# Kernel tuning notes

Hardware: AMD Instinct MI355X
Metric: run time of the kernel (lower is better)

## Reference

```python
import jax, jax.numpy as jnp
import numpy as np
from jax import lax

N, S, F_IN = 50000, 16, 64
HID, HEADS = 128, 4
C = HID // HEADS  # 32
E = 1600000
NEG_SLOPE = 0.2


def setup_inputs() -> dict:
    key = jax.random.key(0)
    ks = jax.random.split(key, 16)
    sc = lambda *sh: 1.0 / np.sqrt(sh[-1])
    inp = {}
    inp['node_features_sequence'] = jax.random.normal(ks[0], (N, S, F_IN), dtype=jnp.float32)
    inp['edge_index'] = jax.random.randint(ks[1], (2, E), 0, N, dtype=jnp.int64)
    # GRU params (single layer, order r,z,n as in torch)
    inp['gru_w_ih'] = jax.random.normal(ks[2], (3 * HID, F_IN), jnp.float32) * sc(F_IN)
    inp['gru_w_hh'] = jax.random.normal(ks[3], (3 * HID, HID), jnp.float32) * sc(HID)
    inp['gru_b_ih'] = jax.random.normal(ks[4], (3 * HID,), jnp.float32) * 0.01
    inp['gru_b_hh'] = jax.random.normal(ks[5], (3 * HID,), jnp.float32) * 0.01
    # GAT layer 1
    inp['gat1_w'] = jax.random.normal(ks[6], (HID, HID), jnp.float32) * sc(HID)
    inp['gat1_a_src'] = jax.random.normal(ks[7], (HEADS, C), jnp.float32) * sc(C)
    inp['gat1_a_dst'] = jax.random.normal(ks[8], (HEADS, C), jnp.float32) * sc(C)
    inp['gat1_b'] = jnp.zeros((HID,), jnp.float32)
    # GAT layer 2
    inp['gat2_w'] = jax.random.normal(ks[9], (HID, HID), jnp.float32) * sc(HID)
    inp['gat2_a_src'] = jax.random.normal(ks[10], (HEADS, C), jnp.float32) * sc(C)
    inp['gat2_a_dst'] = jax.random.normal(ks[11], (HEADS, C), jnp.float32) * sc(C)
    inp['gat2_b'] = jnp.zeros((HID,), jnp.float32)
    # classifier
    inp['clf_w'] = jax.random.normal(ks[12], (1, HID), jnp.float32) * sc(HID)
    inp['clf_b'] = jnp.zeros((1,), jnp.float32)
    return inp


def gru_last(xs, w_ih, w_hh, b_ih, b_hh):
    # xs: [N, S, F] -> last hidden [N, H]
    n, _, _ = xs.shape
    h_dim = w_hh.shape[1]
    gi_all = jnp.einsum('nsf,gf->nsg', xs, w_ih) + b_ih  # [N,S,3H]
    gi_all = jnp.swapaxes(gi_all, 0, 1)  # [S,N,3H]

    def step(h, gi):
        gh = h @ w_hh.T + b_hh
        i_r, i_z, i_n = jnp.split(gi, 3, axis=-1)
        h_r, h_z, h_n = jnp.split(gh, 3, axis=-1)
        r = jax.nn.sigmoid(i_r + h_r)
        z = jax.nn.sigmoid(i_z + h_z)
        nn_ = jnp.tanh(i_n + r * h_n)
        h_new = (1.0 - z) * nn_ + z * h
        return h_new, None

    h0 = jnp.zeros((n, h_dim), xs.dtype)
    h_last, _ = lax.scan(step, h0, gi_all)
    return h_last


def gat_layer(x, src, dst, w, a_src, a_dst, b):
    # x: [N, HID]; PyG GATConv with add_self_loops, concat heads
    n = x.shape[0]
    h = (x @ w.T).reshape(n, HEADS, C)  # [N,H,C]
    a_s = jnp.einsum('nhc,hc->nh', h, a_src)  # [N,H]
    a_d = jnp.einsum('nhc,hc->nh', h, a_dst)
    e = jax.nn.leaky_relu(a_s[src] + a_d[dst], NEG_SLOPE)  # [E',H]
    m = jax.ops.segment_max(e, dst, num_segments=n)
    m = jnp.where(jnp.isfinite(m), m, 0.0)
    ex = jnp.exp(e - m[dst])
    denom = jax.ops.segment_sum(ex, dst, num_segments=n)
    alpha = ex / (denom[dst] + 1e-16)  # [E',H]
    msg = h[src] * alpha[:, :, None]  # [E',H,C]
    out = jax.ops.segment_sum(msg, dst, num_segments=n)  # [N,H,C]
    return out.reshape(n, HEADS * C) + b


def reference(node_features_sequence, edge_index,
              gru_w_ih, gru_w_hh, gru_b_ih, gru_b_hh,
              gat1_w, gat1_a_src, gat1_a_dst, gat1_b,
              gat2_w, gat2_a_src, gat2_a_dst, gat2_b,
              clf_w, clf_b):
    n = node_features_sequence.shape[0]
    # add self loops once (same structure for both layers)
    loops = jnp.arange(n, dtype=edge_index.dtype)
    src = jnp.concatenate([edge_index[0], loops])
    dst = jnp.concatenate([edge_index[1], loops])

    x = gru_last(node_features_sequence, gru_w_ih, gru_w_hh, gru_b_ih, gru_b_hh)
    x = jax.nn.elu(gat_layer(x, src, dst, gat1_w, gat1_a_src, gat1_a_dst, gat1_b))
    x = jax.nn.elu(gat_layer(x, src, dst, gat2_w, gat2_a_src, gat2_a_dst, gat2_b))
    return jax.nn.sigmoid(x @ clf_w.T + clf_b)  # [N,1]
```

## Files before the change

### kernel.cpp

```cpp
#include <hip/hip_runtime.h>
#include <hip/hip_bf16.h>
#include <hip/hip_fp16.h>
#include <math.h>

#define N_NODES 50000
#define NP      50048
#define SEQ     16
#define FIN     64
#define HID     128
#define NEDGE   1600000
#define NB_SCAN 196
#define AGG_CAP 96

typedef __attribute__((ext_vector_type(8))) short short8;
typedef __attribute__((ext_vector_type(4))) float f32x4;

__device__ __forceinline__ float lrelu02(float v) { return v > 0.f ? v : 0.2f * v; }
__device__ __forceinline__ float frcp(float v) { return __builtin_amdgcn_rcpf(v); }
__device__ __forceinline__ float ex2(float v) { return __builtin_amdgcn_exp2f(v); }
__device__ __forceinline__ float sigmoidf_(float v) { return frcp(1.f + __expf(-v)); }
__device__ __forceinline__ float eluf_(float v) { return v > 0.f ? v : (__expf(v) - 1.f); }

__device__ __forceinline__ unsigned bfpk(float lo, float hi) {
    union { __hip_bfloat162 h; unsigned u; } c;
    c.h = __float22bfloat162_rn(make_float2(lo, hi));
    return c.u;
}
__device__ __forceinline__ unsigned hfpk(float lo, float hi) {
    union { __half2 h; unsigned u; } c;
    c.h = __float22half2_rn(make_float2(lo, hi));
    return c.u;
}
__device__ __forceinline__ float2 h2f2(unsigned u) {
    union { unsigned u; __half2 h; } c;
    c.u = u;
    return __half22float2(c.h);
}
__device__ __forceinline__ short8 pack8s(float4 a, float4 b, float s) {
    union { short8 sv; unsigned u[4]; } r;
    r.u[0] = bfpk(a.x * s, a.y * s); r.u[1] = bfpk(a.z * s, a.w * s);
    r.u[2] = bfpk(b.x * s, b.y * s); r.u[3] = bfpk(b.z * s, b.w * s);
    return r.sv;
}

#define BAR() do { asm volatile("s_waitcnt lgkmcnt(0)" ::: "memory"); \
                   __builtin_amdgcn_s_barrier(); } while (0)

__global__ __launch_bounds__(512, 2) void gru_fused(
    const float* __restrict__ x,
    const float* __restrict__ w_ih,
    const float* __restrict__ w_hh,
    const float* __restrict__ b_ih,
    const float* __restrict__ b_hh,
    float* __restrict__ hout)
{
    __shared__ __align__(16) short hA[2][2][32][136];
    __shared__ __align__(16) short xB[2][2][32][72];

    const int tid  = threadIdx.x;
    const int wave = tid >> 6;
    const int lane = tid & 63;
    const int q    = lane >> 4;
    const int rl   = lane & 15;
    const int n0   = blockIdx.x * 64;
    const int ch   = wave * 16 + rl;

    const float S1 = 1.44269504088896341f;
    const float S2 = 2.88539008177792682f;
    short8 whhf[3][4];
    short8 wihf[3][2];
#pragma unroll
    for (int g = 0; g < 3; g++) {
        const float gs = (g == 2) ? S2 : S1;
        int row = g * 128 + ch;
#pragma unroll
        for (int kc = 0; kc < 4; kc++) {
            const float* p = w_hh + row * HID + kc * 32 + q * 8;
            whhf[g][kc] = pack8s(*(const float4*)p, *(const float4*)(p + 4), gs);
        }
#pragma unroll
        for (int kc = 0; kc < 2; kc++) {
            const float* p = w_ih + row * FIN + kc * 32 + q * 8;
            wihf[g][kc] = pack8s(*(const float4*)p, *(const float4*)(p + 4), gs);
        }
    }

    const float br  = (b_ih[ch] + b_hh[ch]) * S1;
    const float bz  = (b_ih[128 + ch] + b_hh[128 + ch]) * S1;
    const float bin = b_ih[256 + ch] * S2;
    const float bhn = b_hh[256 + ch] * S2;

    const int sn = tid >> 4;
    const int sk = (tid & 15) * 4;
    int g0n = n0 + sn;      if (g0n > N_NODES - 1) g0n = N_NODES - 1;
    int g1n = n0 + 32 + sn; if (g1n > N_NODES - 1) g1n = N_NODES - 1;
    const float* xs0 = x + (size_t)g0n * SEQ * FIN + sk;
    const float* xs1 = x + (size_t)g1n * SEQ * FIN + sk;

    float hreg[2][2][4];
#pragma unroll
    for (int g = 0; g < 2; g++)
#pragma unroll
        for (int mt = 0; mt < 2; mt++)
#pragma unroll
            for (int r = 0; r < 4; r++) hreg[g][mt][r] = 0.f;

    f32x4 accr[2][2], accz[2][2], accin[2][2], acchn[2][2];
    float4 xh[2];

    {
        float4 v = *(const float4*)(xs0);
        int2 pv;
        pv.x = (int)bfpk(v.x, v.y);
        pv.y = (int)bfpk(v.z, v.w);
        *(int2*)&xB[0][0][sn][sk] = pv;
    }
    xh[1] = *(const float4*)(xs1);
    BAR();

#define GATE_BLOCK(B, PG, DO_HW, HWB)                                             \
    {                                                                             \
        _Pragma("unroll")                                                         \
        for (int mt = 0; mt < 2; mt++) {                                          \
            float rg[4], zg[4], et[4];                                            \
            _Pragma("unroll")                                                     \
            for (int r = 0; r < 4; r++) {                                         \
                float er  = ex2(fminf(-(accr[B][mt][r] + br), 60.f));             \
                float ezv = ex2(fminf(-(accz[B][mt][r] + bz), 60.f));             \
                float dr = er + 1.f, dz = ezv + 1.f;                              \
                float ip = frcp(dr * dz);                                         \
                rg[r] = dz * ip; zg[r] = dr * ip;                                 \
                float ap = accin[B][mt][r] + bin + rg[r] * (acchn[B][mt][r] + bhn); \
                et[r] = ex2(fminf(ap, 120.f));                                    \
            }                                                                     \
            _Pragma("unroll")                                                     \
            for (int pr = 0; pr < 2; pr++) {                                      \
                float dd0 = et[2 * pr] + 1.f, dd1 = et[2 * pr + 1] + 1.f;         \
                float ipt = frcp(dd0 * dd1);                                      \
                float nn0 = 1.f - 2.f * (ipt * dd1);                              \
                float nn1 = 1.f - 2.f * (ipt * dd0);                              \
                float h0 = zg[2 * pr]     * (hreg[PG][mt][2 * pr]     - nn0) + nn0; \
                float h1 = zg[2 * pr + 1] * (hreg[PG][mt][2 * pr + 1] - nn1) + nn1; \
                hreg[PG][mt][2 * pr] = h0; hreg[PG][mt][2 * pr + 1] = h1;         \
            }                                                                     \
            if (DO_HW) {                                                          \
                unsigned u01 = bfpk(hreg[PG][mt][0], hreg[PG][mt][1]);            \
                unsigned u23 = bfpk(hreg[PG][mt][2], hreg[PG][mt][3]);            \
                const int nb = mt * 16 + q * 4;                                   \
                hA[PG][HWB][nb + 0][ch] = (short)(u01 & 0xFFFF);                  \
                hA[PG][HWB][nb + 1][ch] = (short)(u01 >> 16);                     \
                hA[PG][HWB][nb + 2][ch] = (short)(u23 & 0xFFFF);                  \
                hA[PG][HWB][nb + 3][ch] = (short)(u23 >> 16);                     \
            }                                                                     \
        }                                                                         \
    }

#define GRU_PHASE(G, PG, DO_GATE, HWB, DO_HW, DO_XW, XWB, XPTR)                   \
    {                                                                             \
        short8 xf[2][2], hf[2][4];                                                \
        _Pragma("unroll")                                                         \
        for (int mt = 0; mt < 2; mt++)                                            \
            _Pragma("unroll")                                                     \
            for (int kc = 0; kc < 2; kc++)                                        \
                xf[mt][kc] = *(const short8*)&xB[G][t & 1][mt * 16 + rl][kc * 32 + q * 8]; \
        if (t > 0) {                                                              \
            _Pragma("unroll")                                                     \
            for (int mt = 0; mt < 2; mt++)                                        \
                _Pragma("unroll")                                                 \
                for (int kc = 0; kc < 4; kc++)                                    \
                    hf[mt][kc] = *(const short8*)&hA[G][(t - 1) & 1][mt * 16 + rl][kc * 32 + q * 8]; \
        }                                                                         \
        if (t + 1 < SEQ) xh[G] = *(const float4*)(XPTR + (t + 1) * FIN);          \
        _Pragma("unroll")                                                         \
        for (int mt = 0; mt < 2; mt++) {                                          \
            accr[G][mt]  = __builtin_amdgcn_mfma_f32_16x16x32_bf16(xf[mt][0], wihf[0][0], (f32x4)0.f, 0, 0, 0); \
            accz[G][mt]  = __builtin_amdgcn_mfma_f32_16x16x32_bf16(xf[mt][0], wihf[1][0], (f32x4)0.f, 0, 0, 0); \
            accin[G][mt] = __builtin_amdgcn_mfma_f32_16x16x32_bf16(xf[mt][0], wihf[2][0], (f32x4)0.f, 0, 0, 0); \
            accr[G][mt]  = __builtin_amdgcn_mfma_f32_16x16x32_bf16(xf[mt][1], wihf[0][1], accr[G][mt], 0, 0, 0); \
            accz[G][mt]  = __builtin_amdgcn_mfma_f32_16x16x32_bf16(xf[mt][1], wihf[1][1], accz[G][mt], 0, 0, 0); \
            accin[G][mt] = __builtin_amdgcn_mfma_f32_16x16x32_bf16(xf[mt][1], wihf[2][1], accin[G][mt], 0, 0, 0); \
            if (t > 0) {                                                          \
                acchn[G][mt] = __builtin_amdgcn_mfma_f32_16x16x32_bf16(hf[mt][0], whhf[2][0], (f32x4)0.f, 0, 0, 0); \
                _Pragma("unroll")                                                 \
                for (int kc = 0; kc < 4; kc++) {                                  \
                    accr[G][mt]  = __builtin_amdgcn_mfma_f32_16x16x32_bf16(hf[mt][kc], whhf[0][kc], accr[G][mt], 0, 0, 0);  \
                    accz[G][mt]  = __builtin_amdgcn_mfma_f32_16x16x32_bf16(hf[mt][kc], whhf[1][kc], accz[G][mt], 0, 0, 0);  \
                }                                                                 \
                _Pragma("unroll")                                                 \
                for (int kc = 1; kc < 4; kc++)                                    \
                    acchn[G][mt] = __builtin_amdgcn_mfma_f32_16x16x32_bf16(hf[mt][kc], whhf[2][kc], acchn[G][mt], 0, 0, 0); \
            } else {                                                              \
                acchn[G][mt] = (f32x4)0.f;                                        \
            }                                                                     \
        }                                                                         \
        if (DO_GATE) GATE_BLOCK(PG, PG, DO_HW, HWB);                              \
        if (DO_XW) {                                                              \
            int2 pv;                                                              \
            pv.x = (int)bfpk(xh[PG].x, xh[PG].y);                                 \
            pv.y = (int)bfpk(xh[PG].z, xh[PG].w);                                 \
            *(int2*)&xB[PG][XWB][sn][sk] = pv;                                    \
        }                                                                         \
        BAR();                                                                    \
    }

    for (int t = 0; t < SEQ; t++) {
        GRU_PHASE(0, 1, (t > 0), ((t - 1) & 1), (t > 0), 1, (t & 1), xs0)
        GRU_PHASE(1, 0, 1, (t & 1), (t + 1 < SEQ), (t + 1 < SEQ), ((t + 1) & 1), xs1)
    }
#undef GRU_PHASE

    GATE_BLOCK(1, 1, 0, 0);
#undef GATE_BLOCK

#pragma unroll
    for (int g = 0; g < 2; g++)
#pragma unroll
        for (int mt = 0; mt < 2; mt++)
#pragma unroll
            for (int r = 0; r < 4; r++)
                hout[(size_t)(n0 + g * 32 + mt * 16 + q * 4 + r) * HID + ch] = hreg[g][mt][r];
}

__global__ void prep_weights(const float* __restrict__ g1w, const float* __restrict__ g2w,
                             float* __restrict__ g1T, float* __restrict__ g2T)
{
    int i = blockIdx.x * 256 + threadIdx.x;
    if (i < 128 * 128) {
        int k = i >> 7, g = i & 127;
        g1T[i] = g1w[g * 128 + k];
        g2T[i] = g2w[g * 128 + k];
    }
}

__global__ void count_edges(const int* __restrict__ dst, int* __restrict__ deg, int e)
{
    int i = blockIdx.x * 256 + threadIdx.x;
    if (i < e) atomicAdd(&deg[dst[i]], 1);
}

__device__ __forceinline__ int block_scan_inc(int v)
{
    int tid = threadIdx.x, lane = tid & 63, w = tid >> 6;
#pragma unroll
    for (int off = 1; off < 64; off <<= 1) {
        int tmp = __shfl_up(v, off, 64);
        if (lane >= off) v += tmp;
    }
    __shared__ int wsum[4];
    if (lane == 63) wsum[w] = v;
    __syncthreads();
    int add = 0;
    for (int i = 0; i < w; i++) add += wsum[i];
    return v + add;
}

__global__ void scan_block_sums(const int* __restrict__ deg, int* __restrict__ bsum, int n)
{
    int i = blockIdx.x * 256 + threadIdx.x;
    int v = (i < n) ? deg[i] : 0;
#pragma unroll
    for (int off = 32; off >= 1; off >>= 1) v += __shfl_xor(v, off, 64);
    __shared__ int ws[4];
    if ((threadIdx.x & 63) == 0) ws[threadIdx.x >> 6] = v;
    __syncthreads();
    if (threadIdx.x == 0) bsum[blockIdx.x] = ws[0] + ws[1] + ws[2] + ws[3];
}

__global__ void scan_bsum(int* __restrict__ bsum, int nb)
{
    int tid = threadIdx.x;
    int v = (tid < nb) ? bsum[tid] : 0;
    v = block_scan_inc(v);
    if (tid < nb) bsum[tid] = v;
}

__global__ void scan_final(const int* __restrict__ deg, const int* __restrict__ bsum,
                           int* __restrict__ rp, int n)
{
    int i = blockIdx.x * 256 + threadIdx.x;
    int v = (i < n) ? deg[i] : 0;
    int s = block_scan_inc(v);
    int add = (blockIdx.x > 0) ? bsum[blockIdx.x - 1] : 0;
    if (i < n) rp[i + 1] = s + add;
    if (i == 0) rp[0] = 0;
}

__global__ void fill_edges(const int* __restrict__ src, const int* __restrict__ dst,
                           const int* __restrict__ rp, int* __restrict__ cur,
                           int* __restrict__ col, int e)
{
    int i = blockIdx.x * 256 + threadIdx.x;
    if (i < e) {
        int d = dst[i];
        int pos = atomicAdd(&cur[d], 1);
        col[rp[d] + pos] = src[i];
    }
}

__global__ __launch_bounds__(256) void proj_attn(
    const float* __restrict__ x, const float* __restrict__ wT,
    const float* __restrict__ a_src, const float* __restrict__ a_dst,
    unsigned* __restrict__ hph, float* __restrict__ as_, float* __restrict__ ad_)
{
    __shared__ float xt[32][33];
    __shared__ float wt[32][128];
    __shared__ float ot[32][132];
    const int tid = threadIdx.x;
    const int tx = tid & 7;
    const int ty = tid >> 3;
    const int n0 = blockIdx.x * 32;
    float acc[4][4];
#pragma unroll
    for (int i = 0; i < 4; i++)
#pragma unroll
        for (int j = 0; j < 4; j++) acc[i][j] = 0.f;

    for (int k0 = 0; k0 < 128; k0 += 32) {
        __syncthreads();
#pragma unroll
        for (int i = 0; i < 4; i++) {
            int flat = tid + i * 256;
            int n = flat >> 5, k = flat & 31;
            xt[n][k] = x[(n0 + n) * HID + k0 + k];
        }
#pragma unroll
        for (int i = 0; i < 16; i++) {
            int flat = tid + i * 256;
            int kk = flat >> 7, g = flat & 127;
            wt[kk][g] = wT[(k0 + kk) * HID + g];
        }
        __syncthreads();
#pragma unroll 8
        for (int kk = 0; kk < 32; kk++) {
            float xv[4];
#pragma unroll
            for (int i = 0; i < 4; i++) xv[i] = xt[tx * 4 + i][kk];
            float4 wv = *(const float4*)&wt[kk][ty * 4];
#pragma unroll
            for (int i = 0; i < 4; i++) {
                acc[i][0] = fmaf(xv[i], wv.x, acc[i][0]);
                acc[i][1] = fmaf(xv[i], wv.y, acc[i][1]);
                acc[i][2] = fmaf(xv[i], wv.z, acc[i][2]);
                acc[i][3] = fmaf(xv[i], wv.w, acc[i][3]);
            }
        }
    }
#pragma unroll
    for (int i = 0; i < 4; i++) {
        int node = tx * 4 + i;
        ot[node][ty * 4 + 0] = acc[i][0];
        ot[node][ty * 4 + 1] = acc[i][1];
        ot[node][ty * 4 + 2] = acc[i][2];
        ot[node][ty * 4 + 3] = acc[i][3];
        uint2 pv;
        pv.x = hfpk(acc[i][0], acc[i][1]);
        pv.y = hfpk(acc[i][2], acc[i][3]);
        *(uint2*)&hph[(size_t)(n0 + node) * 64 + ty * 2] = pv;
    }
    __syncthreads();
    if (tid < 128) {
        int node = tid >> 2, head = tid & 3;
        const float* ar = a_src + head * 32;
        const float* br = a_dst + head * 32;
        float s = 0.f, d = 0.f;
#pragma unroll
        for (int j = 0; j < 32; j += 4) {
            float4 hv = *(const float4*)&ot[node][head * 32 + j];
            float4 av = *(const float4*)&ar[j];
            float4 bv = *(const float4*)&br[j];
            s += hv.x * av.x + hv.y * av.y + hv.z * av.z + hv.w * av.w;
            d += hv.x * bv.x + hv.y * bv.y + hv.z * bv.z + hv.w * bv.w;
        }
        as_[(n0 + node) * 4 + head] = s;
        ad_[(n0 + node) * 4 + head] = d;
    }
}

template <bool CLF>
__global__ __launch_bounds__(256) void gat_agg(
    const unsigned* __restrict__ hph, const float* __restrict__ as_,
    const float* __restrict__ ad_, const int* __restrict__ rp,
    const int* __restrict__ col, const float* __restrict__ bias,
    float* __restrict__ out, const float* __restrict__ cw,
    const float* __restrict__ cb, int n_nodes)
{
    __shared__ float exl[4][AGG_CAP][4];
    const int widx = threadIdx.x >> 6;
    const int lane = threadIdx.x & 63;
    const int n = blockIdx.x * 4 + widx;
    if (n >= n_nodes) return;

    const int e0 = rp[n], e1 = rp[n + 1];
    const int deg = e1 - e0;
    float4 adv = *(const float4*)&ad_[n * 4];
    float4 asn = *(const float4*)&as_[n * 4];
    float xs0 = __expf(lrelu02(asn.x + adv.x)), xs1 = __expf(lrelu02(asn.y + adv.y));
    float xs2 = __expf(lrelu02(asn.z + adv.z)), xs3 = __expf(lrelu02(asn.w + adv.w));

    float d0 = 0.f, d1 = 0.f, d2 = 0.f, d3 = 0.f;
    for (int e = e0 + lane; e < e1; e += 64) {
        int s = col[e];
        float4 a = *(const float4*)&as_[s * 4];
        float x0 = __expf(lrelu02(a.x + adv.x));
        float x1 = __expf(lrelu02(a.y + adv.y));
        float x2 = __expf(lrelu02(a.z + adv.z));
        float x3 = __expf(lrelu02(a.w + adv.w));
        int idx = e - e0;
        if (idx < AGG_CAP) {
            exl[widx][idx][0] = x0; exl[widx][idx][1] = x1;
            exl[widx][idx][2] = x2; exl[widx][idx][3] = x3;
        }
        d0 += x0; d1 += x1; d2 += x2; d3 += x3;
    }
#pragma unroll
    for (int off = 32; off >= 1; off >>= 1) {
        d0 += __shfl_xor(d0, off, 64);
        d1 += __shfl_xor(d1, off, 64);
        d2 += __shfl_xor(d2, off, 64);
        d3 += __shfl_xor(d3, off, 64);
    }
    d0 += xs0; d1 += xs1; d2 += xs2; d3 += xs3;
    float i0 = frcp(d0 + 1e-16f), i1 = frcp(d1 + 1e-16f);
    float i2 = frcp(d2 + 1e-16f), i3 = frcp(d3 + 1e-16f);

    const int head = lane >> 4;
    float invh = (head == 0) ? i0 : (head == 1) ? i1 : (head == 2) ? i2 : i3;
    float exsh = (head == 0) ? xs0 : (head == 1) ? xs1 : (head == 2) ? xs2 : xs3;
    float adh  = (head == 0) ? adv.x : (head == 1) ? adv.y : (head == 2) ? adv.z : adv.w;

    float2 sv = h2f2(hph[(size_t)n * 64 + lane]);
    float acc0 = exsh * sv.x;
    float acc1 = exsh * sv.y;

    if (deg <= AGG_CAP) {
        int e = e0;
        for (; e + 4 <= e1; e += 4) {
            int s_[4]; float w_[4]; unsigned u_[4];
#pragma unroll
            for (int u = 0; u < 4; u++) {
                s_[u] = col[e + u];
                w_[u] = exl[widx][e + u - e0][head];
            }
#pragma unroll
            for (int u = 0; u < 4; u++)
                u_[u] = hph[(size_t)s_[u] * 64 + lane];
#pragma unroll
            for (int u = 0; u < 4; u++) {
                float2 f = h2f2(u_[u]);
                acc0 = fmaf(w_[u], f.x, acc0);
                acc1 = fmaf(w_[u], f.y, acc1);
            }
        }
        for (; e < e1; e++) {
            int s = col[e];
            float w = exl[widx][e - e0][head];
            float2 f = h2f2(hph[(size_t)s * 64 + lane]);
            acc0 = fmaf(w, f.x, acc0);
            acc1 = fmaf(w, f.y, acc1);
        }
    } else {
        for (int e = e0; e < e1; e++) {
            int s = col[e];
            int idx = e - e0;
            float w;
            if (idx < AGG_CAP) w = exl[widx][idx][head];
            else               w = __expf(lrelu02(as_[s * 4 + head] + adh));
            float2 f = h2f2(hph[(size_t)s * 64 + lane]);
            acc0 = fmaf(w, f.x, acc0);
            acc1 = fmaf(w, f.y, acc1);
        }
    }

    float2 b2 = *(const float2*)&bias[2 * lane];
    float o0 = eluf_(acc0 * invh + b2.x);
    float o1 = eluf_(acc1 * invh + b2.y);
    if (CLF) {
        float2 cwv = *(const float2*)&cw[2 * lane];
        float v = o0 * cwv.x + o1 * cwv.y;
#pragma unroll
        for (int off = 32; off >= 1; off >>= 1) v += __shfl_xor(v, off, 64);
        if (lane == 0) out[n] = sigmoidf_(v + cb[0]);
    } else {
        *(float2*)&out[(size_t)n * HID + 2 * lane] = make_float2(o0, o1);
    }
}

extern "C" void kernel_launch(void* const* d_in, const int* in_sizes, int n_in,
                              void* d_out, int out_size, void* d_ws, size_t ws_size,
                              hipStream_t stream)
{
    const float* x     = (const float*)d_in[0];
    const int*   ei    = (const int*)d_in[1];
    const float* w_ih  = (const float*)d_in[2];
    const float* w_hh  = (const float*)d_in[3];
    const float* b_ih  = (const float*)d_in[4];
    const float* b_hh  = (const float*)d_in[5];
    const float* g1w   = (const float*)d_in[6];
    const float* g1as  = (const float*)d_in[7];
    const float* g1ad  = (const float*)d_in[8];
    const float* g1b   = (const float*)d_in[9];
    const float* g2w   = (const float*)d_in[10];
    const float* g2as  = (const float*)d_in[11];
    const float* g2ad  = (const float*)d_in[12];
    const float* g2b   = (const float*)d_in[13];
    const float* cw    = (const float*)d_in[14];
    const float* cb    = (const float*)d_in[15];
    float* out = (float*)d_out;

    char* wsb = (char*)d_ws;
    size_t off = 0;
    auto alc = [&](size_t bytes) { size_t o = off; off += (bytes + 255) & ~(size_t)255; return o; };

    float*    bufA = (float*)(wsb + alc((size_t)NP * HID * 4));
    float*    bufC = (float*)(wsb + alc((size_t)NP * HID * 4));
    unsigned* hph  = (unsigned*)(wsb + alc((size_t)NP * 64 * 4));
    float*    as_  = (float*)(wsb + alc((size_t)NP * 4 * 4));
    float*    ad_  = (float*)(wsb + alc((size_t)NP * 4 * 4));
    float*    g1T  = (float*)(wsb + alc((size_t)128 * 128 * 4));
    float*    g2T  = (float*)(wsb + alc((size_t)128 * 128 * 4));
    int*      rp   = (int*)(wsb + alc((size_t)(N_NODES + 1) * 4));
    int*      deg  = (int*)(wsb + alc((size_t)N_NODES * 4));
    int*      cur  = (int*)(wsb + alc((size_t)N_NODES * 4));
    int*      col  = (int*)(wsb + alc((size_t)NEDGE * 4));
    int*      bsum = (int*)(wsb + alc((size_t)256 * 4));

    const int* src = ei;
    const int* dst = ei + NEDGE;

    hipMemsetAsync(deg, 0, (size_t)N_NODES * 4, stream);
    hipMemsetAsync(cur, 0, (size_t)N_NODES * 4, stream);

    prep_weights<<<64, 256, 0, stream>>>(g1w, g2w, g1T, g2T);

    count_edges<<<NEDGE / 256, 256, 0, stream>>>(dst, deg, NEDGE);
    scan_block_sums<<<NB_SCAN, 256, 0, stream>>>(deg, bsum, N_NODES);
    scan_bsum<<<1, 256, 0, stream>>>(bsum, NB_SCAN);
    scan_final<<<NB_SCAN, 256, 0, stream>>>(deg, bsum, rp, N_NODES);
    fill_edges<<<NEDGE / 256, 256, 0, stream>>>(src, dst, rp, cur, col, NEDGE);

    gru_fused<<<NP / 64, 512, 0, stream>>>(x, w_ih, w_hh, b_ih, b_hh, bufA);

    proj_attn<<<NP / 32, 256, 0, stream>>>(bufA, g1T, g1as, g1ad, hph, as_, ad_);
    gat_agg<false><<<(N_NODES + 3) / 4, 256, 0, stream>>>(hph, as_, ad_, rp, col, g1b, bufC,
                                                          nullptr, nullptr, N_NODES);

    proj_attn<<<NP / 32, 256, 0, stream>>>(bufC, g2T, g2as, g2ad, hph, as_, ad_);
    gat_agg<true><<<(N_NODES + 3) / 4, 256, 0, stream>>>(hph, as_, ad_, rp, col, g2b, out,
                                                         cw, cb, N_NODES);
}
```

Before: 828.5 us.

## Use fp16 MFMA in GAT projection and single-pass online softmax aggregation

The GAT projection kernel now converts inputs to fp16 and uses MFMA 16x16x32 instructions with weights read directly in row-major form, so the transpose prep kernel is no longer needed. The aggregation kernel drops the two-pass scheme that cached attention weights in LDS and instead computes each edge weight inline while accumulating numerator and denominator together, then normalizes at the end. This removes one pass over the edge list and the LDS traffic, but recomputes the per-head exp in every lane of the head group and adds fp16 rounding to the projection inputs.

```diff
diff --git a/kernel.cpp b/kernel.cpp
--- a/kernel.cpp
+++ b/kernel.cpp
@@ -10,9 +10,9 @@
 #define HID     128
 #define NEDGE   1600000
 #define NB_SCAN 196
-#define AGG_CAP 96
 
 typedef __attribute__((ext_vector_type(8))) short short8;
+typedef __attribute__((ext_vector_type(8))) _Float16 half8;
 typedef __attribute__((ext_vector_type(4))) float f32x4;
 
 __device__ __forceinline__ float lrelu02(float v) { return v > 0.f ? v : 0.2f * v; }
@@ -41,6 +41,12 @@
     r.u[0] = bfpk(a.x * s, a.y * s); r.u[1] = bfpk(a.z * s, a.w * s);
     r.u[2] = bfpk(b.x * s, b.y * s); r.u[3] = bfpk(b.z * s, b.w * s);
     return r.sv;
+}
+__device__ __forceinline__ half8 pack8h(float4 a, float4 b) {
+    union { half8 hv; unsigned u[4]; } r;
+    r.u[0] = hfpk(a.x, a.y); r.u[1] = hfpk(a.z, a.w);
+    r.u[2] = hfpk(b.x, b.y); r.u[3] = hfpk(b.z, b.w);
+    return r.hv;
 }
 
 #define BAR() do { asm volatile("s_waitcnt lgkmcnt(0)" ::: "memory"); \
@@ -221,17 +227,6 @@
                 hout[(size_t)(n0 + g * 32 + mt * 16 + q * 4 + r) * HID + ch] = hreg[g][mt][r];
 }
 
-__global__ void prep_weights(const float* __restrict__ g1w, const float* __restrict__ g2w,
-                             float* __restrict__ g1T, float* __restrict__ g2T)
-{
-    int i = blockIdx.x * 256 + threadIdx.x;
-    if (i < 128 * 128) {
-        int k = i >> 7, g = i & 127;
-        g1T[i] = g1w[g * 128 + k];
-        g2T[i] = g2w[g * 128 + k];
-    }
-}
-
 __global__ void count_edges(const int* __restrict__ dst, int* __restrict__ deg, int e)
 {
     int i = blockIdx.x * 256 + threadIdx.x;
@@ -298,66 +293,83 @@
 }
 
 __global__ __launch_bounds__(256) void proj_attn(
-    const float* __restrict__ x, const float* __restrict__ wT,
+    const float* __restrict__ x, const float* __restrict__ w,
     const float* __restrict__ a_src, const float* __restrict__ a_dst,
     unsigned* __restrict__ hph, float* __restrict__ as_, float* __restrict__ ad_)
 {
-    __shared__ float xt[32][33];
-    __shared__ float wt[32][128];
-    __shared__ float ot[32][132];
+    __shared__ __align__(16) unsigned short xt[32][136];
+    __shared__ __align__(16) float ot[32][132];
     const int tid = threadIdx.x;
-    const int tx = tid & 7;
-    const int ty = tid >> 3;
+    const int wv = tid >> 6, lane = tid & 63;
+    const int q = lane >> 4, rl = lane & 15;
     const int n0 = blockIdx.x * 32;
-    float acc[4][4];
-#pragma unroll
-    for (int i = 0; i < 4; i++)
-#pragma unroll
-        for (int j = 0; j < 4; j++) acc[i][j] = 0.f;
-
-    for (int k0 = 0; k0 < 128; k0 += 32) {
-        __syncthreads();
-#pragma unroll
-        for (int i = 0; i < 4; i++) {
-            int flat = tid + i * 256;
-            int n = flat >> 5, k = flat & 31;
-            xt[n][k] = x[(n0 + n) * HID + k0 + k];
+
+    half8 wf[2][4];
+#pragma unroll
+    for (int nf = 0; nf < 2; nf++)
+#pragma unroll
+        for (int kc = 0; kc < 4; kc++) {
+            const float* p = w + (32 * wv + nf * 16 + rl) * HID + kc * 32 + q * 8;
+            wf[nf][kc] = pack8h(*(const float4*)p, *(const float4*)(p + 4));
         }
-#pragma unroll
-        for (int i = 0; i < 16; i++) {
-            int flat = tid + i * 256;
-            int kk = flat >> 7, g = flat & 127;
-            wt[kk][g] = wT[(k0 + kk) * HID + g];
-        }
-        __syncthreads();
-#pragma unroll 8
-        for (int kk = 0; kk < 32; kk++) {
-            float xv[4];
-#pragma unroll
-            for (int i = 0; i < 4; i++) xv[i] = xt[tx * 4 + i][kk];
-            float4 wv = *(const float4*)&wt[kk][ty * 4];
-#pragma unroll
-            for (int i = 0; i < 4; i++) {
-                acc[i][0] = fmaf(xv[i], wv.x, acc[i][0]);
-                acc[i][1] = fmaf(xv[i], wv.y, acc[i][1]);
-                acc[i][2] = fmaf(xv[i], wv.z, acc[i][2]);
-                acc[i][3] = fmaf(xv[i], wv.w, acc[i][3]);
-            }
-        }
-    }
-#pragma unroll
-    for (int i = 0; i < 4; i++) {
-        int node = tx * 4 + i;
-        ot[node][ty * 4 + 0] = acc[i][0];
-        ot[node][ty * 4 + 1] = acc[i][1];
-        ot[node][ty * 4 + 2] = acc[i][2];
-        ot[node][ty * 4 + 3] = acc[i][3];
-        uint2 pv;
-        pv.x = hfpk(acc[i][0], acc[i][1]);
-        pv.y = hfpk(acc[i][2], acc[i][3]);
-        *(uint2*)&hph[(size_t)(n0 + node) * 64 + ty * 2] = pv;
+
+    {
+        const int nn = tid >> 3, c0 = (tid & 7) * 16;
+        const float* xp = x + (size_t)(n0 + nn) * HID + c0;
+        float4 v0 = *(const float4*)(xp + 0);
+        float4 v1 = *(const float4*)(xp + 4);
+        float4 v2 = *(const float4*)(xp + 8);
+        float4 v3 = *(const float4*)(xp + 12);
+        uint4 pv;
+        pv.x = hfpk(v0.x, v0.y); pv.y = hfpk(v0.z, v0.w);
+        pv.z = hfpk(v1.x, v1.y); pv.w = hfpk(v1.z, v1.w);
+        *(uint4*)&xt[nn][c0] = pv;
+        pv.x = hfpk(v2.x, v2.y); pv.y = hfpk(v2.z, v2.w);
+        pv.z = hfpk(v3.x, v3.y); pv.w = hfpk(v3.z, v3.w);
+        *(uint4*)&xt[nn][c0 + 8] = pv;
     }
     __syncthreads();
+
+    f32x4 acc[2][2];
+#pragma unroll
+    for (int mt = 0; mt < 2; mt++)
+#pragma unroll
+        for (int nf = 0; nf < 2; nf++) acc[mt][nf] = (f32x4)0.f;
+
+#pragma unroll
+    for (int kc = 0; kc < 4; kc++) {
+        half8 af0 = *(const half8*)&xt[rl][kc * 32 + q * 8];
+        half8 af1 = *(const half8*)&xt[16 + rl][kc * 32 + q * 8];
+        acc[0][0] = __builtin_amdgcn_mfma_f32_16x16x32_f16(af0, wf[0][kc], acc[0][0], 0, 0, 0);
+        acc[0][1] = __builtin_amdgcn_mfma_f32_16x16x32_f16(af0, wf[1][kc], acc[0][1], 0, 0, 0);
+        acc[1][0] = __builtin_amdgcn_mfma_f32_16x16x32_f16(af1, wf[0][kc], acc[1][0], 0, 0, 0);
+        acc[1][1] = __builtin_amdgcn_mfma_f32_16x16x32_f16(af1, wf[1][kc], acc[1][1], 0, 0, 0);
+    }
+
+#pragma unroll
+    for (int mt = 0; mt < 2; mt++)
+#pragma unroll
+        for (int nf = 0; nf < 2; nf++)
+#pragma unroll
+            for (int r = 0; r < 4; r++)
+                ot[mt * 16 + q * 4 + r][32 * wv + nf * 16 + rl] = acc[mt][nf][r];
+    __syncthreads();
+
+    {
+        const int nn = tid >> 3, c0 = (tid & 7) * 16;
+        float4 v0 = *(const float4*)&ot[nn][c0];
+        float4 v1 = *(const float4*)&ot[nn][c0 + 4];
+        float4 v2 = *(const float4*)&ot[nn][c0 + 8];
+        float4 v3 = *(const float4*)&ot[nn][c0 + 12];
+        uint4 pv;
+        pv.x = hfpk(v0.x, v0.y); pv.y = hfpk(v0.z, v0.w);
+        pv.z = hfpk(v1.x, v1.y); pv.w = hfpk(v1.z, v1.w);
+        *(uint4*)&hph[(size_t)(n0 + nn) * 64 + c0 / 2] = pv;
+        pv.x = hfpk(v2.x, v2.y); pv.y = hfpk(v2.z, v2.w);
+        pv.z = hfpk(v3.x, v3.y); pv.w = hfpk(v3.z, v3.w);
+        *(uint4*)&hph[(size_t)(n0 + nn) * 64 + c0 / 2 + 4] = pv;
+    }
+
     if (tid < 128) {
         int node = tid >> 2, head = tid & 3;
         const float* ar = a_src + head * 32;
@@ -384,93 +396,54 @@
     float* __restrict__ out, const float* __restrict__ cw,
     const float* __restrict__ cb, int n_nodes)
 {
-    __shared__ float exl[4][AGG_CAP][4];
-    const int widx = threadIdx.x >> 6;
     const int lane = threadIdx.x & 63;
-    const int n = blockIdx.x * 4 + widx;
+    const int n = blockIdx.x * 4 + (threadIdx.x >> 6);
     if (n >= n_nodes) return;
 
     const int e0 = rp[n], e1 = rp[n + 1];
-    const int deg = e1 - e0;
-    float4 adv = *(const float4*)&ad_[n * 4];
-    float4 asn = *(const float4*)&as_[n * 4];
-    float xs0 = __expf(lrelu02(asn.x + adv.x)), xs1 = __expf(lrelu02(asn.y + adv.y));
-    float xs2 = __expf(lrelu02(asn.z + adv.z)), xs3 = __expf(lrelu02(asn.w + adv.w));
-
-    float d0 = 0.f, d1 = 0.f, d2 = 0.f, d3 = 0.f;
-    for (int e = e0 + lane; e < e1; e += 64) {
+    const int head = lane >> 4;
+    const float adh = ad_[n * 4 + head];
+
+    float wself = __expf(lrelu02(as_[n * 4 + head] + adh));
+    float2 sv = h2f2(hph[(size_t)n * 64 + lane]);
+    float den = wself;
+    float acc0 = wself * sv.x;
+    float acc1 = wself * sv.y;
+
+    int e = e0;
+    for (; e + 4 <= e1; e += 4) {
+        int s0 = col[e], s1 = col[e + 1], s2 = col[e + 2], s3 = col[e + 3];
+        float a0 = as_[s0 * 4 + head];
+        float a1 = as_[s1 * 4 + head];
+        float a2 = as_[s2 * 4 + head];
+        float a3 = as_[s3 * 4 + head];
+        unsigned u0 = hph[(size_t)s0 * 64 + lane];
+        unsigned u1 = hph[(size_t)s1 * 64 + lane];
+        unsigned u2 = hph[(size_t)s2 * 64 + lane];
+        unsigned u3 = hph[(size_t)s3 * 64 + lane];
+        float w0 = __expf(lrelu02(a0 + adh));
+        float w1 = __expf(lrelu02(a1 + adh));
+        float w2 = __expf(lrelu02(a2 + adh));
+        float w3 = __expf(lrelu02(a3 + adh));
+        float2 f0 = h2f2(u0), f1 = h2f2(u1), f2 = h2f2(u2), f3 = h2f2(u3);
+        den += w0 + w1 + w2 + w3;
+        acc0 = fmaf(w0, f0.x, acc0); acc1 = fmaf(w0, f0.y, acc1);
+        acc0 = fmaf(w1, f1.x, acc0); acc1 = fmaf(w1, f1.y, acc1);
+        acc0 = fmaf(w2, f2.x, acc0); acc1 = fmaf(w2, f2.y, acc1);
+        acc0 = fmaf(w3, f3.x, acc0); acc1 = fmaf(w3, f3.y, acc1);
+    }
+    for (; e < e1; e++) {
         int s = col[e];
-        float4 a = *(const float4*)&as_[s * 4];
-        float x0 = __expf(lrelu02(a.x + adv.x));
-        float x1 = __expf(lrelu02(a.y + adv.y));
-        float x2 = __expf(lrelu02(a.z + adv.z));
-        float x3 = __expf(lrelu02(a.w + adv.w));
-        int idx = e - e0;
-        if (idx < AGG_CAP) {
-            exl[widx][idx][0] = x0; exl[widx][idx][1] = x1;
-            exl[widx][idx][2] = x2; exl[widx][idx][3] = x3;
-        }
-        d0 += x0; d1 += x1; d2 += x2; d3 += x3;
-    }
-#pragma unroll
-    for (int off = 32; off >= 1; off >>= 1) {
-        d0 += __shfl_xor(d0, off, 64);
-        d1 += __shfl_xor(d1, off, 64);
-        d2 += __shfl_xor(d2, off, 64);
-        d3 += __shfl_xor(d3, off, 64);
-    }
-    d0 += xs0; d1 += xs1; d2 += xs2; d3 += xs3;
-    float i0 = frcp(d0 + 1e-16f), i1 = frcp(d1 + 1e-16f);
-    float i2 = frcp(d2 + 1e-16f), i3 = frcp(d3 + 1e-16f);
-
-    const int head = lane >> 4;
-    float invh = (head == 0) ? i0 : (head == 1) ? i1 : (head == 2) ? i2 : i3;
-    float exsh = (head == 0) ? xs0 : (head == 1) ? xs1 : (head == 2) ? xs2 : xs3;
-    float adh  = (head == 0) ? adv.x : (head == 1) ? adv.y : (head == 2) ? adv.z : adv.w;
-
-    float2 sv = h2f2(hph[(size_t)n * 64 + lane]);
-    float acc0 = exsh * sv.x;
-    float acc1 = exsh * sv.y;
-
-    if (deg <= AGG_CAP) {
-        int e = e0;
-        for (; e + 4 <= e1; e += 4) {
-            int s_[4]; float w_[4]; unsigned u_[4];
-#pragma unroll
-            for (int u = 0; u < 4; u++) {
-                s_[u] = col[e + u];
-                w_[u] = exl[widx][e + u - e0][head];
-            }
-#pragma unroll
-            for (int u = 0; u < 4; u++)
-                u_[u] = hph[(size_t)s_[u] * 64 + lane];
-#pragma unroll
-            for (int u = 0; u < 4; u++) {
-                float2 f = h2f2(u_[u]);
-                acc0 = fmaf(w_[u], f.x, acc0);
-                acc1 = fmaf(w_[u], f.y, acc1);
-            }
-        }
-        for (; e < e1; e++) {
-            int s = col[e];
-            float w = exl[widx][e - e0][head];
-            float2 f = h2f2(hph[(size_t)s * 64 + lane]);
-            acc0 = fmaf(w, f.x, acc0);
-            acc1 = fmaf(w, f.y, acc1);
-        }
-    } else {
-        for (int e = e0; e < e1; e++) {
-            int s = col[e];
-            int idx = e - e0;
-            float w;
-            if (idx < AGG_CAP) w = exl[widx][idx][head];
-            else               w = __expf(lrelu02(as_[s * 4 + head] + adh));
-            float2 f = h2f2(hph[(size_t)s * 64 + lane]);
-            acc0 = fmaf(w, f.x, acc0);
-            acc1 = fmaf(w, f.y, acc1);
-        }
-    }
-
+        float a = as_[s * 4 + head];
+        unsigned u = hph[(size_t)s * 64 + lane];
+        float w = __expf(lrelu02(a + adh));
+        float2 f = h2f2(u);
+        den += w;
+        acc0 = fmaf(w, f.x, acc0);
+        acc1 = fmaf(w, f.y, acc1);
+    }
+
+    float invh = frcp(den + 1e-16f);
     float2 b2 = *(const float2*)&bias[2 * lane];
     float o0 = eluf_(acc0 * invh + b2.x);
     float o1 = eluf_(acc1 * invh + b2.y);
@@ -516,8 +489,6 @@
     unsigned* hph  = (unsigned*)(wsb + alc((size_t)NP * 64 * 4));
     float*    as_  = (float*)(wsb + alc((size_t)NP * 4 * 4));
     float*    ad_  = (float*)(wsb + alc((size_t)NP * 4 * 4));
-    float*    g1T  = (float*)(wsb + alc((size_t)128 * 128 * 4));
-    float*    g2T  = (float*)(wsb + alc((size_t)128 * 128 * 4));
     int*      rp   = (int*)(wsb + alc((size_t)(N_NODES + 1) * 4));
     int*      deg  = (int*)(wsb + alc((size_t)N_NODES * 4));
     int*      cur  = (int*)(wsb + alc((size_t)N_NODES * 4));
@@ -530,8 +501,6 @@
     hipMemsetAsync(deg, 0, (size_t)N_NODES * 4, stream);
     hipMemsetAsync(cur, 0, (size_t)N_NODES * 4, stream);
 
-    prep_weights<<<64, 256, 0, stream>>>(g1w, g2w, g1T, g2T);
-
     count_edges<<<NEDGE / 256, 256, 0, stream>>>(dst, deg, NEDGE);
     scan_block_sums<<<NB_SCAN, 256, 0, stream>>>(deg, bsum, N_NODES);
     scan_bsum<<<1, 256, 0, stream>>>(bsum, NB_SCAN);
@@ -540,11 +509,11 @@
 
     gru_fused<<<NP / 64, 512, 0, stream>>>(x, w_ih, w_hh, b_ih, b_hh, bufA);
 
-    proj_attn<<<NP / 32, 256, 0, stream>>>(bufA, g1T, g1as, g1ad, hph, as_, ad_);
+    proj_attn<<<NP / 32, 256, 0, stream>>>(bufA, g1w, g1as, g1ad, hph, as_, ad_);
     gat_agg<false><<<(N_NODES + 3) / 4, 256, 0, stream>>>(hph, as_, ad_, rp, col, g1b, bufC,
                                                           nullptr, nullptr, N_NODES);
 
-    proj_attn<<<NP / 32, 256, 0, stream>>>(bufC, g2T, g2as, g2ad, hph, as_, ad_);
+    proj_attn<<<NP / 32, 256, 0, stream>>>(bufC, g2w, g2as, g2ad, hph, as_, ad_);
     gat_agg<true><<<(N_NODES + 3) / 4, 256, 0, stream>>>(hph, as_, ad_, rp, col, g2b, out,
                                                          cw, cb, N_NODES);
 }
```

Measured after the change: 802.6 us. 1.03x faster.
